# Kernel tuning notes

Hardware: AMD Instinct MI355X
Metric: run time of the kernel (lower is better)

Reference implementation:

```python
import jax, jax.numpy as jnp
import numpy as np

F_FACETS = 400000
TEX_PER = 4            # textures per facet (counts sum must equal total textures)
T_TEX = F_FACETS * TEX_PER
C_IN = 64
C_OUT = 64
L = 2
N_BASIS = (L + 1) ** 2  # 9
BN_EPS = 1e-3


def setup_inputs() -> dict:
    key = jax.random.key(0)
    k1, k2, k3 = jax.random.split(key, 3)
    input_texture = jax.random.normal(k1, (T_TEX, C_IN), jnp.float32)
    bary_coeff = jax.random.uniform(k2, (T_TEX, N_BASIS), jnp.float32)
    # per-facet texture counts; constant 4 so counts sum exactly to T_TEX
    num_texture = jnp.full((F_FACETS,), TEX_PER, dtype=jnp.int32)
    # xavier_normal_ on [O, I, K]: fan_in = I*K, fan_out = ... torch uses fan_in=I*K? For 3D it treats dim1*rest.
    std = float(np.sqrt(2.0 / (C_IN * N_BASIS + C_OUT * N_BASIS)))
    weights = jax.random.normal(k3, (C_OUT, C_IN, N_BASIS), jnp.float32) * std
    biases = jnp.zeros((1, C_OUT), jnp.float32)
    gamma = jnp.ones((C_OUT,), jnp.float32)
    beta = jnp.zeros((C_OUT,), jnp.float32)
    return {
        "input_texture": input_texture,
        "bary_coeff": bary_coeff,
        "weights": weights,
        "biases": biases,
        "gamma": gamma,
        "beta": beta,
        "num_texture": num_texture,
    }


def reference(input_texture, bary_coeff, weights, biases, gamma, beta, num_texture):
    T = input_texture.shape[0]
    n_facets = num_texture.shape[0]
    n_basis = weights.shape[2]
    # per-texture contribution: contrib[t,o] = sum_{i,k} x[t,i] * W[o,i,k] * bary[t,k]
    # loop over small fixed basis count (9) to avoid a [T, I, K] intermediate
    contrib = jnp.zeros((T, weights.shape[0]), dtype=input_texture.dtype)
    for k in range(n_basis):
        contrib = contrib + (input_texture @ weights[:, :, k].T) * bary_coeff[:, k:k + 1]
    # scatter-sum per facet (ragged groups given by num_texture), then average
    seg_ids = jnp.repeat(jnp.arange(n_facets), num_texture, total_repeat_length=T)
    facet_sum = jax.ops.segment_sum(contrib, seg_ids, num_segments=n_facets)
    out = facet_sum / num_texture[:, None].astype(facet_sum.dtype)
    # bias + ReLU
    out = jax.nn.relu(out + biases)
    # BatchNorm1d in training mode: batch stats (biased variance), eps=1e-3
    mu = jnp.mean(out, axis=0)
    var = jnp.mean(jnp.square(out - mu), axis=0)
    out = (out - mu) * jax.lax.rsqrt(var + BN_EPS) * gamma + beta
    return out
```

## Files before the change

### kernel.cpp

```cpp
#include <hip/hip_runtime.h>


typedef _Float16 half8  __attribute__((ext_vector_type(8)));
typedef _Float16 h2     __attribute__((ext_vector_type(2)));
typedef __fp16   fp16x2 __attribute__((ext_vector_type(2)));
typedef float    f32x4  __attribute__((ext_vector_type(4)));

#define NGROUPS 100000
#define NPAIRS  50000
#define FFACETS 400000
#define GRID1   768
#define LDSP    9472

#define WAITV(N) asm volatile("s_waitcnt vmcnt(" #N ")" ::: "memory")
#define WAITL0() asm volatile("s_waitcnt lgkmcnt(0)" ::: "memory")
#define FENCE()  asm volatile("" ::: "memory")
#define SB0()    __builtin_amdgcn_sched_barrier(0)

union HF { h2 h[4]; half8 v; };

static __device__ __forceinline__ h2 pkrtz(float a, float b) {
    fp16x2 r = __builtin_amdgcn_cvt_pkrtz(a, b);
    return __builtin_bit_cast(h2, r);
}

static __device__ __forceinline__ void gload16(const void* g, void* l) {
    __builtin_amdgcn_global_load_lds((const __attribute__((address_space(1))) void*)g,
                                     (__attribute__((address_space(3))) void*)l, 16, 0, 0);
}

__global__ __launch_bounds__(256) void prep_kernel(const float* __restrict__ W,
                                                   _Float16* __restrict__ wswz,
                                                   float* __restrict__ stats) {
    int idx = blockIdx.x * 256 + threadIdx.x;
    if (idx < 36864) {
        int j    = idx & 7;
        int lane = (idx >> 3) & 63;
        int mt   = (idx >> 9) & 3;
        int c    = idx >> 11;
        int o    = mt * 16 + (lane & 15);
        int i    = (c & 1) * 32 + ((lane >> 4) << 3) + j;
        int kb   = c >> 1;
        wswz[idx] = (_Float16)W[(o * 64 + i) * 9 + kb];
    }
    if (idx < 128) stats[idx] = 0.0f;
}

__global__ __launch_bounds__(256, 3) void pass1_kernel(
    const float* __restrict__ X, const float* __restrict__ BARY,
    const _Float16* __restrict__ WSWZ, const float* __restrict__ BIAS,
    const int* __restrict__ NTEX, float* __restrict__ OUT,
    float* __restrict__ stats) {

    __shared__ __align__(16) char lds[2][LDSP];
    __shared__ float sl_s[64];
    __shared__ float sl_s2[64];

    const int tid  = threadIdx.x;
    const int wave = tid >> 6;
    const int lane = tid & 63;
    const int col  = lane & 15;
    const int quad = lane >> 4;

    half8 wf[18];
#pragma unroll
    for (int c = 0; c < 18; ++c)
        wf[c] = *(const half8*)(WSWZ + ((size_t)(c * 4 + wave) * 64 + lane) * 8);

    const f32x4 biasv = *(const f32x4*)(BIAS + wave * 16 + quad * 4);

    const int pphys  = (wave << 10) + (lane << 4);
    const int xsoff  = pphys ^ (((pphys >> 8) & 7) << 4);
    const char* Xb   = (const char*)X;
    const char* BAb  = (const char*)BARY;
    const char* NTb  = (const char*)NTEX;

    const int m    = (col & 7) << 4;
    const int a00  = (col << 8) + ((quad << 5) ^ m);
    const int a10  = (col << 8) + (((quad << 5) | 16) ^ m);
    const int bco  = 8192 + col * 36;
    const int nco  = 9344 + ((col >> 2) << 2);

    float sacc[4]  = {0.f, 0.f, 0.f, 0.f};
    float s2acc[4] = {0.f, 0.f, 0.f, 0.f};

    const int b = blockIdx.x;
    const int n = (NPAIRS - 1 - b) / GRID1 + 1;

    auto STAGE = [&](int p, int u) {
        const char* xs = Xb + (size_t)u * 8192;
        gload16(xs + xsoff,        &lds[p][pphys]);
        gload16(xs + 4096 + xsoff, &lds[p][4096 + pphys]);
        gload16(BAb + (size_t)u * 1152 + lane * 16, &lds[p][8192 + lane * 16]);
        if (lane < 8) gload16(BAb + (size_t)u * 1152 + 1024 + lane * 16, &lds[p][9216 + lane * 16]);
        if (lane < 2) gload16(NTb + (size_t)u * 32 + lane * 16,          &lds[p][9344 + lane * 16]);
    };

    auto EPI = [&](f32x4 acc, float rc, int f) {
        f32x4 vv;
#pragma unroll
        for (int r = 0; r < 4; ++r) {
            float s = acc[r];
            s += __shfl_xor(s, 1);
            s += __shfl_xor(s, 2);
            s = s * rc + biasv[r];
            s = s > 0.f ? s : 0.f;
            vv[r] = s;
            sacc[r]  += s;
            s2acc[r] += s * s;
        }
        if ((col & 3) == 0)
            *(f32x4*)(OUT + (size_t)f * 64 + wave * 16 + quad * 4) = vv;
    };

    auto ITER = [&](int p, int u, int upre, bool do_stage) {
        __builtin_amdgcn_s_barrier();
        FENCE();
        const char* L = lds[p];
        f32x4 r0[4], r1[4];
        r0[0] = *(const f32x4*)(L + a00);
        r0[1] = *(const f32x4*)(L + a10);
        r0[2] = *(const f32x4*)(L + a00 + 128);
        r0[3] = *(const f32x4*)(L + a10 + 128);
        r1[0] = *(const f32x4*)(L + 4096 + a00);
        r1[1] = *(const f32x4*)(L + 4096 + a10);
        r1[2] = *(const f32x4*)(L + 4096 + a00 + 128);
        r1[3] = *(const f32x4*)(L + 4096 + a10 + 128);
        float bF0[9], bF1[9];
#pragma unroll
        for (int k = 0; k < 9; ++k) bF0[k] = *(const float*)(L + bco + k * 4);
#pragma unroll
        for (int k = 0; k < 9; ++k) bF1[k] = *(const float*)(L + bco + 576 + k * 4);
        const int nt0 = *(const int*)(L + nco);
        const int nt1 = *(const int*)(L + nco + 16);

        h2 xh0[8], xh1[8], bh0[9], bh1[9];
        xh0[0] = pkrtz(r0[0][0], r0[0][1]);  xh0[1] = pkrtz(r0[0][2], r0[0][3]);
        xh0[2] = pkrtz(r0[1][0], r0[1][1]);  xh0[3] = pkrtz(r0[1][2], r0[1][3]);
        xh0[4] = pkrtz(r0[2][0], r0[2][1]);  xh0[5] = pkrtz(r0[2][2], r0[2][3]);
        xh0[6] = pkrtz(r0[3][0], r0[3][1]);  xh0[7] = pkrtz(r0[3][2], r0[3][3]);
        xh1[0] = pkrtz(r1[0][0], r1[0][1]);  xh1[1] = pkrtz(r1[0][2], r1[0][3]);
        xh1[2] = pkrtz(r1[1][0], r1[1][1]);  xh1[3] = pkrtz(r1[1][2], r1[1][3]);
        xh1[4] = pkrtz(r1[2][0], r1[2][1]);  xh1[5] = pkrtz(r1[2][2], r1[2][3]);
        xh1[6] = pkrtz(r1[3][0], r1[3][1]);  xh1[7] = pkrtz(r1[3][2], r1[3][3]);
#pragma unroll
        for (int k = 0; k < 9; ++k) { bh0[k] = pkrtz(bF0[k], bF0[k]); bh1[k] = pkrtz(bF1[k], bF1[k]); }
        const float rc0 = __builtin_amdgcn_rcpf((float)nt0);
        const float rc1 = __builtin_amdgcn_rcpf((float)nt1);

        WAITL0();
        SB0();
        __builtin_amdgcn_s_barrier();
        FENCE();
        if (do_stage) STAGE(p, upre);
        FENCE();

        f32x4 accA = {0.f, 0.f, 0.f, 0.f};
        f32x4 accB = {0.f, 0.f, 0.f, 0.f};
        __builtin_amdgcn_s_setprio(1);
#pragma unroll
        for (int c = 0; c < 18; ++c) {
            const int hh = (c & 1) * 4;
            const h2 bkA = bh0[c >> 1];
            const h2 bkB = bh1[c >> 1];
            HF fa, fb;
            fa.h[0] = xh0[hh + 0] * bkA;  fa.h[1] = xh0[hh + 1] * bkA;
            fa.h[2] = xh0[hh + 2] * bkA;  fa.h[3] = xh0[hh + 3] * bkA;
            accA = __builtin_amdgcn_mfma_f32_16x16x32_f16(wf[c], fa.v, accA, 0, 0, 0);
            fb.h[0] = xh1[hh + 0] * bkB;  fb.h[1] = xh1[hh + 1] * bkB;
            fb.h[2] = xh1[hh + 2] * bkB;  fb.h[3] = xh1[hh + 3] * bkB;
            accB = __builtin_amdgcn_mfma_f32_16x16x32_f16(wf[c], fb.v, accB, 0, 0, 0);
        }
        __builtin_amdgcn_s_setprio(0);

        const int f0 = u * 8 + (col >> 2);
        EPI(accA, rc0, f0);
        EPI(accB, rc1, f0 + 4);
    };

    STAGE(0, b);
    STAGE(1, b + GRID1);
    WAITV(5); ITER(0, b,         b + 2 * GRID1, true);
    WAITV(7); ITER(1, b + GRID1, b + 3 * GRID1, true);
    int t = 2;
    for (; t < n - 2; ++t) {
        WAITV(9);
        ITER(t & 1, b + t * GRID1, b + (t + 2) * GRID1, true);
    }
    WAITV(9); ITER(t & 1, b + t * GRID1, 0, false); ++t;
    WAITV(4); ITER(t & 1, b + t * GRID1, 0, false);

#pragma unroll
    for (int r = 0; r < 4; ++r) {
        float s = sacc[r], s2 = s2acc[r];
        s  += __shfl_xor(s, 1);  s  += __shfl_xor(s, 2);
        s  += __shfl_xor(s, 4);  s  += __shfl_xor(s, 8);
        s2 += __shfl_xor(s2, 1); s2 += __shfl_xor(s2, 2);
        s2 += __shfl_xor(s2, 4); s2 += __shfl_xor(s2, 8);
        if (col == 0) {
            sl_s [wave * 16 + quad * 4 + r] = s  * 0.25f;
            sl_s2[wave * 16 + quad * 4 + r] = s2 * 0.25f;
        }
    }
    __syncthreads();
    if (tid < 64)        atomicAdd(&stats[tid],      sl_s [tid]);
    else if (tid < 128)  atomicAdd(&stats[tid],      sl_s2[tid - 64]);
}

__global__ __launch_bounds__(256) void pass3_kernel(float* __restrict__ OUT,
    const float* __restrict__ stats, const float* __restrict__ gamma,
    const float* __restrict__ beta) {
    const int tid = threadIdx.x;
    const size_t l = (size_t)blockIdx.x * 256 + tid;
    const int c0 = ((int)l & 15) * 4;
    float mu[4], sc[4], be[4];
    const float invF = 1.0f / (float)FFACETS;
#pragma unroll
    for (int u = 0; u < 4; ++u) {
        int ch = c0 + u;
        float m  = stats[ch] * invF;
        float va = stats[64 + ch] * invF - m * m;
        mu[u] = m;
        sc[u] = rsqrtf(va + 1e-3f) * gamma[ch];
        be[u] = beta[ch];
    }
    const size_t n4 = (size_t)FFACETS * 16;
    for (size_t i = l; i < n4; i += (size_t)gridDim.x * 256) {
        f32x4 v = ((f32x4*)OUT)[i];
#pragma unroll
        for (int u = 0; u < 4; ++u)
            v[u] = (v[u] - mu[u]) * sc[u] + be[u];
        ((f32x4*)OUT)[i] = v;
    }
}

extern "C" void kernel_launch(void* const* d_in, const int* in_sizes, int n_in,
                              void* d_out, int out_size, void* d_ws, size_t ws_size,
                              hipStream_t stream) {
    const float* X     = (const float*)d_in[0];
    const float* BARY  = (const float*)d_in[1];
    const float* W     = (const float*)d_in[2];
    const float* BIAS  = (const float*)d_in[3];
    const float* GAMMA = (const float*)d_in[4];
    const float* BETA  = (const float*)d_in[5];
    const int*   NTEX  = (const int*)d_in[6];
    float* OUT = (float*)d_out;

    _Float16* wswz = (_Float16*)d_ws;
    float* stats   = (float*)((char*)d_ws + 73728);

    prep_kernel<<<144, 256, 0, stream>>>(W, wswz, stats);
    pass1_kernel<<<GRID1, 256, 0, stream>>>(X, BARY, wswz, BIAS, NTEX, OUT, stats);
    pass3_kernel<<<2048, 256, 0, stream>>>(OUT, stats, GAMMA, BETA);
}
```

Baseline: 674.4 us.

## Triple-buffer LDS staging to drop the second barrier per iteration

```diff
diff --git a/kernel.cpp b/kernel.cpp
--- a/kernel.cpp
+++ b/kernel.cpp
@@ -13,11 +13,9 @@
 #define LDSP    9472
 
 #define WAITV(N) asm volatile("s_waitcnt vmcnt(" #N ")" ::: "memory")
-#define WAITL0() asm volatile("s_waitcnt lgkmcnt(0)" ::: "memory")
 #define FENCE()  asm volatile("" ::: "memory")
-#define SB0()    __builtin_amdgcn_sched_barrier(0)
-
-union HF { h2 h[4]; half8 v; };
+
+union H8 { h2 h[4]; half8 v; };
 
 static __device__ __forceinline__ h2 pkrtz(float a, float b) {
     fp16x2 r = __builtin_amdgcn_cvt_pkrtz(a, b);
@@ -52,7 +50,7 @@
     const int* __restrict__ NTEX, float* __restrict__ OUT,
     float* __restrict__ stats) {
 
-    __shared__ __align__(16) char lds[2][LDSP];
+    __shared__ __align__(16) char ldsbuf[3 * LDSP];
     __shared__ float sl_s[64];
     __shared__ float sl_s2[64];
 
@@ -69,17 +67,16 @@
 
     const f32x4 biasv = *(const f32x4*)(BIAS + wave * 16 + quad * 4);
 
-    const int pphys  = (wave << 10) + (lane << 4);
-    const int xsoff  = pphys ^ (((pphys >> 8) & 7) << 4);
-    const char* Xb   = (const char*)X;
-    const char* BAb  = (const char*)BARY;
-    const char* NTb  = (const char*)NTEX;
-
-    const int m    = (col & 7) << 4;
-    const int a00  = (col << 8) + ((quad << 5) ^ m);
-    const int a10  = (col << 8) + (((quad << 5) | 16) ^ m);
-    const int bco  = 8192 + col * 36;
-    const int nco  = 9344 + ((col >> 2) << 2);
+    const int xdst = (wave << 10) + (lane << 4);
+    const int xsrc = ((lane & 15) << 8) + ((lane >> 4) << 5)
+                   + ((wave & 1) << 4) + ((wave >> 1) << 7);
+    const char* Xb  = (const char*)X;
+    const char* BAb = (const char*)BARY;
+    const char* NTb = (const char*)NTEX;
+
+    const int xrd = lane << 4;
+    const int bco = 8192 + col * 36;
+    const int nco = 9344 + ((col >> 2) << 2);
 
     float sacc[4]  = {0.f, 0.f, 0.f, 0.f};
     float s2acc[4] = {0.f, 0.f, 0.f, 0.f};
@@ -87,13 +84,15 @@
     const int b = blockIdx.x;
     const int n = (NPAIRS - 1 - b) / GRID1 + 1;
 
-    auto STAGE = [&](int p, int u) {
+    auto STAGE = [&](char* S, int u) {
         const char* xs = Xb + (size_t)u * 8192;
-        gload16(xs + xsoff,        &lds[p][pphys]);
-        gload16(xs + 4096 + xsoff, &lds[p][4096 + pphys]);
-        gload16(BAb + (size_t)u * 1152 + lane * 16, &lds[p][8192 + lane * 16]);
-        if (lane < 8) gload16(BAb + (size_t)u * 1152 + 1024 + lane * 16, &lds[p][9216 + lane * 16]);
-        if (lane < 2) gload16(NTb + (size_t)u * 32 + lane * 16,          &lds[p][9344 + lane * 16]);
+        FENCE();
+        gload16(xs + xsrc,        S + xdst);
+        gload16(xs + 4096 + xsrc, S + 4096 + xdst);
+        gload16(BAb + (size_t)u * 1152 + lane * 16, S + 8192 + lane * 16);
+        if (lane < 8) gload16(BAb + (size_t)u * 1152 + 1024 + lane * 16, S + 9216 + lane * 16);
+        if (lane < 2) gload16(NTb + (size_t)u * 32 + lane * 16,          S + 9344 + lane * 16);
+        FENCE();
     };
 
     auto EPI = [&](f32x4 acc, float rc, int f) {
@@ -113,19 +112,15 @@
             *(f32x4*)(OUT + (size_t)f * 64 + wave * 16 + quad * 4) = vv;
     };
 
-    auto ITER = [&](int p, int u, int upre, bool do_stage) {
+    auto ITER = [&](const char* L, char* S, int u, int upre, bool do_stage) {
         __builtin_amdgcn_s_barrier();
         FENCE();
-        const char* L = lds[p];
         f32x4 r0[4], r1[4];
-        r0[0] = *(const f32x4*)(L + a00);
-        r0[1] = *(const f32x4*)(L + a10);
-        r0[2] = *(const f32x4*)(L + a00 + 128);
-        r0[3] = *(const f32x4*)(L + a10 + 128);
-        r1[0] = *(const f32x4*)(L + 4096 + a00);
-        r1[1] = *(const f32x4*)(L + 4096 + a10);
-        r1[2] = *(const f32x4*)(L + 4096 + a00 + 128);
-        r1[3] = *(const f32x4*)(L + 4096 + a10 + 128);
+#pragma unroll
+        for (int j = 0; j < 4; ++j) {
+            r0[j] = *(const f32x4*)(L + (j << 10) + xrd);
+            r1[j] = *(const f32x4*)(L + 4096 + (j << 10) + xrd);
+        }
         float bF0[9], bF1[9];
 #pragma unroll
         for (int k = 0; k < 9; ++k) bF0[k] = *(const float*)(L + bco + k * 4);
@@ -133,6 +128,8 @@
         for (int k = 0; k < 9; ++k) bF1[k] = *(const float*)(L + bco + 576 + k * 4);
         const int nt0 = *(const int*)(L + nco);
         const int nt1 = *(const int*)(L + nco + 16);
+
+        if (do_stage) STAGE(S, upre);
 
         h2 xh0[8], xh1[8], bh0[9], bh1[9];
         xh0[0] = pkrtz(r0[0][0], r0[0][1]);  xh0[1] = pkrtz(r0[0][2], r0[0][3]);
@@ -148,13 +145,6 @@
         const float rc0 = __builtin_amdgcn_rcpf((float)nt0);
         const float rc1 = __builtin_amdgcn_rcpf((float)nt1);
 
-        WAITL0();
-        SB0();
-        __builtin_amdgcn_s_barrier();
-        FENCE();
-        if (do_stage) STAGE(p, upre);
-        FENCE();
-
         f32x4 accA = {0.f, 0.f, 0.f, 0.f};
         f32x4 accB = {0.f, 0.f, 0.f, 0.f};
         __builtin_amdgcn_s_setprio(1);
@@ -163,7 +153,7 @@
             const int hh = (c & 1) * 4;
             const h2 bkA = bh0[c >> 1];
             const h2 bkB = bh1[c >> 1];
-            HF fa, fb;
+            H8 fa, fb;
             fa.h[0] = xh0[hh + 0] * bkA;  fa.h[1] = xh0[hh + 1] * bkA;
             fa.h[2] = xh0[hh + 2] * bkA;  fa.h[3] = xh0[hh + 3] * bkA;
             accA = __builtin_amdgcn_mfma_f32_16x16x32_f16(wf[c], fa.v, accA, 0, 0, 0);
@@ -178,17 +168,24 @@
         EPI(accB, rc1, f0 + 4);
     };
 
-    STAGE(0, b);
-    STAGE(1, b + GRID1);
-    WAITV(5); ITER(0, b,         b + 2 * GRID1, true);
-    WAITV(7); ITER(1, b + GRID1, b + 3 * GRID1, true);
+    char* B0 = ldsbuf;
+    char* B1 = ldsbuf + LDSP;
+    char* B2 = ldsbuf + 2 * LDSP;
+
+    STAGE(B0, b);
+    STAGE(B1, b + GRID1);
+    WAITV(5); ITER(B0, B2, b,         b + 2 * GRID1, true);
+    WAITV(7); ITER(B1, B0, b + GRID1, b + 3 * GRID1, true);
+    char *rd = B2, *st = B1, *ot = B0;
     int t = 2;
     for (; t < n - 2; ++t) {
         WAITV(9);
-        ITER(t & 1, b + t * GRID1, b + (t + 2) * GRID1, true);
-    }
-    WAITV(9); ITER(t & 1, b + t * GRID1, 0, false); ++t;
-    WAITV(4); ITER(t & 1, b + t * GRID1, 0, false);
+        ITER(rd, st, b + t * GRID1, b + (t + 2) * GRID1, true);
+        char* tmp = ot; ot = st; st = rd; rd = tmp;
+    }
+    WAITV(9); ITER(rd, st, b + t * GRID1, 0, false);
+    { char* tmp = ot; ot = st; st = rd; rd = tmp; } ++t;
+    WAITV(4); ITER(rd, st, b + t * GRID1, 0, false);
 
 #pragma unroll
     for (int r = 0; r < 4; ++r) {
```

Result: no change. 666.0 us (-1.2%).
